# Performance work log

Hardware: AMD Instinct MI355X
Metric: run time of the kernel (lower is better)

The kernel has to match this reference:

```python
import jax, jax.numpy as jnp
import numpy as np

B, S, E, H, D = 4, 2048, 2048, 16, 128
EPS = 1e-6


def _rope_cache(seq_len, dim, base=10000.0):
    # standard rotary cache, half-split layout matching rotate_half
    inv_freq = 1.0 / (base ** (np.arange(0, dim // 2, dtype=np.float32) / (dim // 2)))
    t = np.arange(seq_len, dtype=np.float32)
    freqs = np.outer(t, inv_freq)                     # [S, D/2]
    emb = np.concatenate([freqs, freqs], axis=-1)     # [S, D]
    cos = jnp.asarray(np.cos(emb))[None, :, None, :]  # [1, S, 1, D]
    sin = jnp.asarray(np.sin(emb))[None, :, None, :]
    return cos, sin


def setup_inputs() -> dict:
    key = jax.random.key(0)
    ks = jax.random.split(key, 5)
    scale = 1.0 / np.sqrt(E)
    x = jax.random.normal(ks[0], (B, S, E), dtype=jnp.float32)
    Wq = jax.random.normal(ks[1], (E, E), dtype=jnp.float32) * scale
    Wk = jax.random.normal(ks[2], (E, E), dtype=jnp.float32) * scale
    Wv = jax.random.normal(ks[3], (E, E), dtype=jnp.float32) * scale
    Wo = jax.random.normal(ks[4], (E, E), dtype=jnp.float32) * scale
    cos, sin = _rope_cache(S, D)
    return {"x": x, "cos": cos, "sin": sin, "Wq": Wq, "Wk": Wk, "Wv": Wv, "Wo": Wo}


def _rotate_half(t):
    d = t.shape[-1] // 2
    return jnp.concatenate([-t[..., d:], t[..., :d]], axis=-1)


def _rms_norm(t, eps):
    return t * jax.lax.rsqrt(jnp.mean(t * t, axis=-1, keepdims=True) + eps)


def reference(x, cos, sin, Wq, Wk, Wv, Wo):
    b, s, _ = x.shape
    # QKV projections (Linear without bias: x @ W.T), reshape to heads
    q = (x @ Wq.T).reshape(b, s, H, D)
    k = (x @ Wk.T).reshape(b, s, H, D)
    v = (x @ Wv.T).reshape(b, s, H, D)
    # RoPE then QK RMSNorm (no learned scale)
    q = _rms_norm(q * cos + _rotate_half(q) * sin, EPS)
    k = _rms_norm(k * cos + _rotate_half(k) * sin, EPS)
    # non-causal SDPA
    scores = jnp.einsum("bqhd,bkhd->bhqk", q, k) / np.sqrt(D)
    probs = jax.nn.softmax(scores, axis=-1)
    y = jnp.einsum("bhqk,bkhd->bqhd", probs, v).reshape(b, s, H * D)
    return y @ Wo.T
```

## Files before the change

kernel.cpp:

```cpp
#include <hip/hip_runtime.h>
#include <hip/hip_bf16.h>
#include <math.h>


typedef __bf16 bf16_t;
typedef __bf16 bf16x2 __attribute__((ext_vector_type(2)));
typedef __bf16 bf16x4 __attribute__((ext_vector_type(4)));
typedef __bf16 bf16x8 __attribute__((ext_vector_type(8)));
typedef float f32x2 __attribute__((ext_vector_type(2)));
typedef float f32x4 __attribute__((ext_vector_type(4)));
typedef float f32x16 __attribute__((ext_vector_type(16)));
typedef unsigned int u32;
typedef u32 u32x4 __attribute__((ext_vector_type(4)));

typedef __attribute__((address_space(1))) const void gas_cvoid;
typedef __attribute__((address_space(3))) void las_void;

#define MFMA16(a, b, c) __builtin_amdgcn_mfma_f32_16x16x32_bf16((a), (b), (c), 0, 0, 0)
#define MFMA32(a, b, c) __builtin_amdgcn_mfma_f32_32x32x16_bf16((a), (b), (c), 0, 0, 0)

__device__ __forceinline__ void gload16(const void* g, void* l) {
  __builtin_amdgcn_global_load_lds((gas_cvoid*)g, (las_void*)l, 16, 0, 0);
}
__device__ __forceinline__ void pl32(u32& a, u32& b) {
  asm volatile("v_permlane32_swap_b32 %0, %1" : "+v"(a), "+v"(b));
}
__device__ __forceinline__ float fexp2(float x) {
  float r;
  asm("v_exp_f32 %0, %1" : "=v"(r) : "v"(x));
  return r;
}

__global__ __launch_bounds__(256) void cvt_all(const float* __restrict__ x,
                                               const float* __restrict__ w0,
                                               const float* __restrict__ w1,
                                               const float* __restrict__ w2,
                                               const float* __restrict__ w3,
                                               bf16_t* __restrict__ xo,
                                               bf16_t* __restrict__ o0,
                                               bf16_t* __restrict__ o1,
                                               bf16_t* __restrict__ o2,
                                               bf16_t* __restrict__ o3) {
  const float* in;
  bf16_t* out;
  size_t i;
  if (blockIdx.x < 16384) {
    in = x; out = xo;
    i = ((size_t)blockIdx.x * 256 + threadIdx.x) * 4;
  } else {
    const int which = (blockIdx.x - 16384) >> 12;
    in = which == 0 ? w0 : which == 1 ? w1 : which == 2 ? w2 : w3;
    out = which == 0 ? o0 : which == 1 ? o1 : which == 2 ? o2 : o3;
    i = ((size_t)((blockIdx.x - 16384) & 4095) * 256 + threadIdx.x) * 4;
  }
  f32x4 v = *(const f32x4*)&in[i];
  bf16x4 o;
#pragma unroll
  for (int j = 0; j < 4; ++j) o[j] = (bf16_t)v[j];
  *(bf16x4*)&out[i] = o;
}

__global__ __launch_bounds__(512, 2) void gemm_qkv(const bf16_t* __restrict__ xb,
                                                   const bf16_t* __restrict__ Wq,
                                                   const bf16_t* __restrict__ Wk,
                                                   const bf16_t* __restrict__ Wv,
                                                   bf16_t* __restrict__ Qo,
                                                   bf16_t* __restrict__ Ko,
                                                   bf16_t* __restrict__ Vo) {
  constexpr int K = 2048;
  __shared__ __attribute__((aligned(16))) char lds[131072];
  const int tid = threadIdx.x;
  const int wave = tid >> 6, lane = tid & 63;
  const int seg = blockIdx.x >> 8;
  const int sbid = blockIdx.x & 255;
  const int swz = (sbid & 7) * 32 + (sbid >> 3);
  const int NT = (seg == 2) ? 32 : 8;
  const int m0 = (swz / NT) * 256, n0 = (swz % NT) * 256;
  const bf16_t* A = (seg == 2) ? Wv : xb;
  const bf16_t* Bt = (seg == 0) ? Wq : (seg == 1) ? Wk : xb;
  bf16_t* C = (seg == 0) ? Qo : (seg == 1) ? Ko : Vo;

  const int srow = tid >> 3;
  const int scol = ((tid & 7) ^ (srow & 7)) * 8;
  const bf16_t* aBase = A + (size_t)(m0 + srow) * K + scol;
  const bf16_t* bBase = Bt + (size_t)(n0 + srow) * K + scol;

  const int wm = wave >> 2, wn = wave & 3;
  const int l15 = lane & 15, l4 = lane >> 4;
  const int axor = l15 & 7;
  char* const wdst = lds + wave * 1024;

  f32x4 acc[8][4] = {};

  gload16(bBase, wdst + 32768);
  gload16(bBase + (size_t)64 * K, wdst + 32768 + 8192);
  gload16(bBase + (size_t)128 * K, wdst + 32768 + 16384);
  gload16(bBase + (size_t)192 * K, wdst + 32768 + 24576);
  gload16(aBase, wdst);
  gload16(aBase + (size_t)128 * K, wdst + 16384);
  gload16(aBase + (size_t)64 * K, wdst + 8192);
  gload16(aBase + (size_t)192 * K, wdst + 24576);

  for (int t = 0; t < 32; ++t) {
    const int buf = t & 1, nbuf = buf ^ 1;
    const char* la = lds + buf * 65536 + wm * 16384;
    const char* lb = lds + buf * 65536 + 32768 + (wn >> 1) * 16384 + (wn & 1) * 8192;
    char* const ndst = wdst + nbuf * 65536;
    bf16x8 bF[4][2];
#pragma unroll
    for (int q = 0; q < 4; ++q) {
      if (q == 0) {
        asm volatile("s_waitcnt vmcnt(2)" ::: "memory");
      } else if (q == 2) {
        if (t < 31)
          asm volatile("s_waitcnt vmcnt(4)" ::: "memory");
        else
          asm volatile("s_waitcnt vmcnt(0)" ::: "memory");
      }
      __builtin_amdgcn_s_barrier();

      bf16x8 aF[2][2];
#pragma unroll
      for (int dm = 0; dm < 2; ++dm)
#pragma unroll
        for (int kk = 0; kk < 2; ++kk)
          aF[dm][kk] = *(const bf16x8*)(la + ((q * 2 + dm) * 16 + l15) * 128 +
                                        ((kk * 4 + l4) ^ axor) * 16);
      if (q == 0) {
#pragma unroll
        for (int ni = 0; ni < 4; ++ni)
#pragma unroll
          for (int kk = 0; kk < 2; ++kk)
            bF[ni][kk] = *(const bf16x8*)(lb + (ni * 16 + l15) * 128 +
                                          ((kk * 4 + l4) ^ axor) * 16);
      }
      if (t < 31) {
        const int off = (t + 1) * 64;
        if (q == 0) {
          gload16(bBase + off, ndst + 32768);
          gload16(bBase + (size_t)64 * K + off, ndst + 32768 + 8192);
        } else if (q == 1) {
          gload16(bBase + (size_t)128 * K + off, ndst + 32768 + 16384);
          gload16(bBase + (size_t)192 * K + off, ndst + 32768 + 24576);
        } else if (q == 2) {
          gload16(aBase + off, ndst);
          gload16(aBase + (size_t)128 * K + off, ndst + 16384);
        } else {
          gload16(aBase + (size_t)64 * K + off, ndst + 8192);
          gload16(aBase + (size_t)192 * K + off, ndst + 24576);
        }
      }
      __builtin_amdgcn_s_setprio(1);
#pragma unroll
      for (int kk = 0; kk < 2; ++kk)
#pragma unroll
        for (int dm = 0; dm < 2; ++dm)
#pragma unroll
          for (int ni = 0; ni < 4; ++ni)
            acc[q * 2 + dm][ni] = MFMA16(aF[dm][kk], bF[ni][kk], acc[q * 2 + dm][ni]);
      __builtin_amdgcn_s_setprio(0);
    }
  }

  const int rBase = m0 + wm * 128 + l4 * 4;
  const int cBase = n0 + wn * 64 + l15;
#pragma unroll
  for (int mi = 0; mi < 8; ++mi)
#pragma unroll
    for (int ni = 0; ni < 4; ++ni)
#pragma unroll
      for (int j = 0; j < 4; ++j) {
        const int r = rBase + mi * 16 + j;
        const int c = cBase + ni * 16;
        const bf16_t v = (bf16_t)acc[mi][ni][j];
        if (seg < 2) {
          const int b = r >> 11, s = r & 2047, hh = c >> 7, d = c & 127;
          C[(((size_t)(b * 16 + hh)) * 2048 + s) * 128 + d] = v;
        } else {
          const int hh = r >> 7, dd = r & 127, b = c >> 11, s = c & 2047;
          C[((size_t)(b * 16 + hh) * 128 + dd) * 2048 + s] = v;
        }
      }
}

__global__ __launch_bounds__(512, 2) void gemm_out(const bf16_t* __restrict__ A,
                                                   const bf16_t* __restrict__ Bt,
                                                   float* __restrict__ C) {
  constexpr int K = 2048;
  __shared__ __attribute__((aligned(16))) char lds[131072];
  const int tid = threadIdx.x;
  const int wave = tid >> 6, lane = tid & 63;
  const int bid = blockIdx.x;
  const int swz = (bid & 7) * 32 + (bid >> 3);
  const int m0 = (swz / 8) * 256, n0 = (swz % 8) * 256;

  const int srow = tid >> 3;
  const int scol = ((tid & 7) ^ (srow & 7)) * 8;
  const bf16_t* aBase = A + (size_t)(m0 + srow) * K + scol;
  const bf16_t* bBase = Bt + (size_t)(n0 + srow) * K + scol;

  const int wm = wave >> 2, wn = wave & 3;
  const int l15 = lane & 15, l4 = lane >> 4;
  const int axor = l15 & 7;
  char* const wdst = lds + wave * 1024;

  f32x4 acc[8][4] = {};

  gload16(bBase, wdst + 32768);
  gload16(bBase + (size_t)64 * K, wdst + 32768 + 8192);
  gload16(bBase + (size_t)128 * K, wdst + 32768 + 16384);
  gload16(bBase + (size_t)192 * K, wdst + 32768 + 24576);
  gload16(aBase, wdst);
  gload16(aBase + (size_t)128 * K, wdst + 16384);
  gload16(aBase + (size_t)64 * K, wdst + 8192);
  gload16(aBase + (size_t)192 * K, wdst + 24576);

  for (int t = 0; t < 32; ++t) {
    const int buf = t & 1, nbuf = buf ^ 1;
    const char* la = lds + buf * 65536 + wm * 16384;
    const char* lb = lds + buf * 65536 + 32768 + (wn >> 1) * 16384 + (wn & 1) * 8192;
    char* const ndst = wdst + nbuf * 65536;
    bf16x8 bF[4][2];
#pragma unroll
    for (int q = 0; q < 4; ++q) {
      if (q == 0) {
        asm volatile("s_waitcnt vmcnt(2)" ::: "memory");
      } else if (q == 2) {
        if (t < 31)
          asm volatile("s_waitcnt vmcnt(4)" ::: "memory");
        else
          asm volatile("s_waitcnt vmcnt(0)" ::: "memory");
      }
      __builtin_amdgcn_s_barrier();

      bf16x8 aF[2][2];
#pragma unroll
      for (int dm = 0; dm < 2; ++dm)
#pragma unroll
        for (int kk = 0; kk < 2; ++kk)
          aF[dm][kk] = *(const bf16x8*)(la + ((q * 2 + dm) * 16 + l15) * 128 +
                                        ((kk * 4 + l4) ^ axor) * 16);
      if (q == 0) {
#pragma unroll
        for (int ni = 0; ni < 4; ++ni)
#pragma unroll
          for (int kk = 0; kk < 2; ++kk)
            bF[ni][kk] = *(const bf16x8*)(lb + (ni * 16 + l15) * 128 +
                                          ((kk * 4 + l4) ^ axor) * 16);
      }
      if (t < 31) {
        const int off = (t + 1) * 64;
        if (q == 0) {
          gload16(bBase + off, ndst + 32768);
          gload16(bBase + (size_t)64 * K + off, ndst + 32768 + 8192);
        } else if (q == 1) {
          gload16(bBase + (size_t)128 * K + off, ndst + 32768 + 16384);
          gload16(bBase + (size_t)192 * K + off, ndst + 32768 + 24576);
        } else if (q == 2) {
          gload16(aBase + off, ndst);
          gload16(aBase + (size_t)128 * K + off, ndst + 16384);
        } else {
          gload16(aBase + (size_t)64 * K + off, ndst + 8192);
          gload16(aBase + (size_t)192 * K + off, ndst + 24576);
        }
      }
      __builtin_amdgcn_s_setprio(1);
#pragma unroll
      for (int kk = 0; kk < 2; ++kk)
#pragma unroll
        for (int dm = 0; dm < 2; ++dm)
#pragma unroll
          for (int ni = 0; ni < 4; ++ni)
            acc[q * 2 + dm][ni] = MFMA16(aF[dm][kk], bF[ni][kk], acc[q * 2 + dm][ni]);
      __builtin_amdgcn_s_setprio(0);
    }
  }

  const int rBase = m0 + wm * 128 + l4 * 4;
  const int cBase = n0 + wn * 64 + l15;
#pragma unroll
  for (int mi = 0; mi < 8; ++mi)
#pragma unroll
    for (int ni = 0; ni < 4; ++ni)
#pragma unroll
      for (int j = 0; j < 4; ++j)
        C[(size_t)(rBase + mi * 16 + j) * 2048 + cBase + ni * 16] = acc[mi][ni][j];
}

__global__ __launch_bounds__(256) void rope_rms2(bf16_t* __restrict__ Qb,
                                                 bf16_t* __restrict__ Kb,
                                                 const float* __restrict__ Cs,
                                                 const float* __restrict__ Sn) {
  bf16_t* T = (blockIdx.x >> 12) ? Kb : Qb;
  const int bid = blockIdx.x & 4095;
  const int wave = threadIdx.x >> 6, lane = threadIdx.x & 63;
#pragma unroll 1
  for (int rr = 0; rr < 8; ++rr) {
    const size_t row = (size_t)bid * 32 + wave * 8 + rr;
    const int s = (int)(row & 2047);
    bf16_t* p = &T[row * 128 + 2 * lane];
    const float a0 = (float)p[0], a1 = (float)p[1];
    f32x2 cv = *(const f32x2*)&Cs[(size_t)s * 128 + 2 * lane];
    f32x2 sv = *(const f32x2*)&Sn[(size_t)s * 128 + 2 * lane];
    const float p0 = __shfl_xor(a0, 32);
    const float p1 = __shfl_xor(a1, 32);
    const float sg = (lane < 32) ? -1.f : 1.f;
    const float r0 = a0 * cv.x + sg * p0 * sv.x;
    const float r1 = a1 * cv.y + sg * p1 * sv.y;
    float ss = r0 * r0 + r1 * r1;
#pragma unroll
    for (int off = 1; off < 64; off <<= 1) ss += __shfl_xor(ss, off);
    const float inv = rsqrtf(ss * (1.0f / 128.0f) + 1e-6f);
    p[0] = (bf16_t)(r0 * inv);
    p[1] = (bf16_t)(r1 * inv);
  }
}

__global__ __launch_bounds__(512, 2) void attn_fwd(const bf16_t* __restrict__ Q,
                                                   const bf16_t* __restrict__ K,
                                                   const bf16_t* __restrict__ Vt,
                                                   bf16_t* __restrict__ Y) {
  __shared__ __attribute__((aligned(16))) bf16_t ldsK[2][64 * 128];
  __shared__ __attribute__((aligned(16))) bf16_t ldsV[2][128 * 64];
  const int tid = threadIdx.x, wave = tid >> 6, lane = tid & 63;
  const int l31 = lane & 31, hi = lane >> 5;
  const int pid = blockIdx.x;
  const int bh = (pid & 7) * 8 + ((pid >> 3) & 7);
  const int qb = pid >> 6;
  const int b = bh >> 4, h = bh & 15;
  const bf16_t* Qh = Q + (size_t)bh * 2048 * 128;
  const bf16_t* Kh = K + (size_t)bh * 2048 * 128;
  const bf16_t* Vh = Vt + (size_t)bh * 128 * 2048;
  const int q0 = qb * 256 + wave * 32;

  bf16x8 qf[8];
#pragma unroll
  for (int dk = 0; dk < 8; ++dk)
    qf[dk] = *(const bf16x8*)&Qh[(size_t)(q0 + l31) * 128 + dk * 16 + hi * 8];

  f32x16 ot[4] = {};
  float l_r = 0.f;
  const float SC2 = 0.08838834764831845f * 1.44269504088896341f;
  const float NC2 = -11.5f * 1.44269504088896341f;

  auto stage = [&](int kt, int bu) {
#pragma unroll
    for (int i = 0; i < 2; ++i) {
      const int G = wave * 64 + lane + i * 512;
      char* dstK = (char*)&ldsK[bu][0] + (wave * 64 + i * 512) * 16;
      char* dstV = (char*)&ldsV[bu][0] + (wave * 64 + i * 512) * 16;
      const int kvr = G >> 4, glk = G & 15;
      gload16(Kh + (size_t)(kt * 64 + kvr) * 128 + ((glk ^ (kvr & 7)) * 8), dstK);
      const int dr = G >> 3, glv = G & 7;
      gload16(Vh + (size_t)dr * 2048 + kt * 64 + ((glv ^ (dr & 7)) * 8), dstV);
    }
  };

  stage(0, 0);
  stage(1, 1);
  asm volatile("s_waitcnt vmcnt(4)" ::: "memory");
  __builtin_amdgcn_s_barrier();
  __builtin_amdgcn_sched_barrier(0);

  for (int kt = 0; kt < 32; ++kt) {
    const int bu = kt & 1;
    const int r7 = l31 & 7;

    f32x16 sa0 = {}, sa1 = {};
    __builtin_amdgcn_s_setprio(1);
#pragma unroll
    for (int dk = 0; dk < 8; ++dk) {
      const int g = ((dk << 1) | hi) ^ r7;
      bf16x8 kf0 = *(const bf16x8*)&ldsK[bu][l31 * 128 + g * 8];
      bf16x8 kf1 = *(const bf16x8*)&ldsK[bu][(32 + l31) * 128 + g * 8];
      sa0 = MFMA32(kf0, qf[dk], sa0);
      sa1 = MFMA32(kf1, qf[dk], sa1);
    }
    __builtin_amdgcn_s_setprio(0);

    u32 w[2][8];
    float ssum = 0.f;
#pragma unroll
    for (int i = 0; i < 8; ++i) {
      const float p0 = fexp2(fmaf(sa0[2 * i], SC2, NC2));
      const float p1 = fexp2(fmaf(sa0[2 * i + 1], SC2, NC2));
      const float p2 = fexp2(fmaf(sa1[2 * i], SC2, NC2));
      const float p3 = fexp2(fmaf(sa1[2 * i + 1], SC2, NC2));
      ssum += (p0 + p1) + (p2 + p3);
      bf16x2 t0, t1;
      t0[0] = (bf16_t)p0; t0[1] = (bf16_t)p1;
      t1[0] = (bf16_t)p2; t1[1] = (bf16_t)p3;
      w[0][i] = __builtin_bit_cast(u32, t0);
      w[1][i] = __builtin_bit_cast(u32, t1);
    }
    ssum += __shfl_xor(ssum, 32);
    l_r += ssum;

#pragma unroll
    for (int ks = 0; ks < 4; ++ks) {
      const int tsel = ks >> 1, k4 = (ks & 1) * 4;
      u32 a0 = w[tsel][k4 + 0], b0 = w[tsel][k4 + 2];
      u32 a1 = w[tsel][k4 + 1], b1 = w[tsel][k4 + 3];
      pl32(a0, b0);
      pl32(a1, b1);
      u32x4 fw;
      fw.x = a0; fw.y = a1; fw.z = b0; fw.w = b1;
      const bf16x8 pf = __builtin_bit_cast(bf16x8, fw);
      const int gv = ((ks << 1) | hi) ^ r7;
      __builtin_amdgcn_s_setprio(1);
#pragma unroll
      for (int db = 0; db < 4; ++db) {
        bf16x8 vf = *(const bf16x8*)&ldsV[bu][(db * 32 + l31) * 64 + gv * 8];
        ot[db] = MFMA32(vf, pf, ot[db]);
      }
      __builtin_amdgcn_s_setprio(0);
    }

    __builtin_amdgcn_s_barrier();
    __builtin_amdgcn_sched_barrier(0);
    if (kt < 30) {
      stage(kt + 2, bu);
      asm volatile("s_waitcnt vmcnt(4)" ::: "memory");
    } else {
      asm volatile("s_waitcnt vmcnt(0)" ::: "memory");
    }
    __builtin_amdgcn_s_barrier();
    __builtin_amdgcn_sched_barrier(0);
  }

  const float rl = 1.f / l_r;
  const size_t yrow = ((size_t)(b * 2048 + q0 + l31) * 16 + h) * 128;
#pragma unroll
  for (int db = 0; db < 4; ++db)
#pragma unroll
    for (int g2 = 0; g2 < 4; ++g2) {
      bf16x4 ov;
#pragma unroll
      for (int j = 0; j < 4; ++j) ov[j] = (bf16_t)(ot[db][g2 * 4 + j] * rl);
      *(bf16x4*)&Y[yrow + db * 32 + g2 * 8 + hi * 4] = ov;
    }
}

extern "C" void kernel_launch(void* const* d_in, const int* in_sizes, int n_in,
                              void* d_out, int out_size, void* d_ws, size_t ws_size,
                              hipStream_t stream) {
  const float* x = (const float*)d_in[0];
  const float* cs = (const float*)d_in[1];
  const float* sn = (const float*)d_in[2];
  const float* Wq = (const float*)d_in[3];
  const float* Wk = (const float*)d_in[4];
  const float* Wv = (const float*)d_in[5];
  const float* Wo = (const float*)d_in[6];

  bf16_t* ws = (bf16_t*)d_ws;
  const size_t TSZ = (size_t)4 * 2048 * 2048;
  const size_t WSZ = (size_t)2048 * 2048;
  bf16_t* xb = ws;
  bf16_t* Wqb = ws + TSZ;
  bf16_t* Wkb = Wqb + WSZ;
  bf16_t* Wvb = Wkb + WSZ;
  bf16_t* Wob = Wvb + WSZ;
  bf16_t* Qb = ws + 2 * TSZ;
  bf16_t* Kb = Qb + TSZ;
  bf16_t* Vtb = Kb + TSZ;
  bf16_t* Yb = xb;

  cvt_all<<<32768, 256, 0, stream>>>(x, Wq, Wk, Wv, Wo, xb, Wqb, Wkb, Wvb, Wob);
  gemm_qkv<<<768, 512, 0, stream>>>(xb, Wqb, Wkb, Wvb, Qb, Kb, Vtb);
  rope_rms2<<<8192, 256, 0, stream>>>(Qb, Kb, cs, sn);
  attn_fwd<<<512, 512, 0, stream>>>(Qb, Kb, Vtb, Yb);
  gemm_out<<<256, 512, 0, stream>>>(Yb, Wob, (float*)d_out);
}
```

Measured before the change: 470.9 us.

## Process two query tiles per wave to reuse staged K/V tiles

Each wave now computes two 32-row query tiles against every staged K/V tile, doubling the queries per block and halving the attention grid. This cuts global-to-LDS K/V traffic and barrier overhead per unit of work. It doubles the Q fragments and output accumulators held in registers, risking spills or lower occupancy, and leaves one block per CU.

```diff
diff --git a/kernel.cpp b/kernel.cpp
--- a/kernel.cpp
+++ b/kernel.cpp
@@ -331,15 +331,17 @@
   const bf16_t* Qh = Q + (size_t)bh * 2048 * 128;
   const bf16_t* Kh = K + (size_t)bh * 2048 * 128;
   const bf16_t* Vh = Vt + (size_t)bh * 128 * 2048;
-  const int q0 = qb * 256 + wave * 32;
-
-  bf16x8 qf[8];
-#pragma unroll
-  for (int dk = 0; dk < 8; ++dk)
-    qf[dk] = *(const bf16x8*)&Qh[(size_t)(q0 + l31) * 128 + dk * 16 + hi * 8];
-
-  f32x16 ot[4] = {};
-  float l_r = 0.f;
+  const int q0 = qb * 512 + wave * 32;
+
+  bf16x8 qfA[8], qfB[8];
+#pragma unroll
+  for (int dk = 0; dk < 8; ++dk) {
+    qfA[dk] = *(const bf16x8*)&Qh[(size_t)(q0 + l31) * 128 + dk * 16 + hi * 8];
+    qfB[dk] = *(const bf16x8*)&Qh[(size_t)(q0 + 256 + l31) * 128 + dk * 16 + hi * 8];
+  }
+
+  f32x16 otA[4] = {}, otB[4] = {};
+  float lA = 0.f, lB = 0.f;
   const float SC2 = 0.08838834764831845f * 1.44269504088896341f;
   const float NC2 = -11.5f * 1.44269504088896341f;
 
@@ -356,16 +358,8 @@
     }
   };
 
-  stage(0, 0);
-  stage(1, 1);
-  asm volatile("s_waitcnt vmcnt(4)" ::: "memory");
-  __builtin_amdgcn_s_barrier();
-  __builtin_amdgcn_sched_barrier(0);
-
-  for (int kt = 0; kt < 32; ++kt) {
-    const int bu = kt & 1;
-    const int r7 = l31 & 7;
-
+  auto tile_work = [&](const bf16x8 (&qf)[8], f32x16 (&ot)[4], float& lr,
+                       int bu, int r7) {
     f32x16 sa0 = {}, sa1 = {};
     __builtin_amdgcn_s_setprio(1);
 #pragma unroll
@@ -394,7 +388,7 @@
       w[1][i] = __builtin_bit_cast(u32, t1);
     }
     ssum += __shfl_xor(ssum, 32);
-    l_r += ssum;
+    lr += ssum;
 
 #pragma unroll
     for (int ks = 0; ks < 4; ++ks) {
@@ -415,6 +409,21 @@
       }
       __builtin_amdgcn_s_setprio(0);
     }
+  };
+
+  stage(0, 0);
+  stage(1, 1);
+  asm volatile("s_waitcnt vmcnt(4)" ::: "memory");
+  __builtin_amdgcn_s_barrier();
+  __builtin_amdgcn_sched_barrier(0);
+
+  for (int kt = 0; kt < 32; ++kt) {
+    const int bu = kt & 1;
+    const int r7 = l31 & 7;
+
+    tile_work(qfA, otA, lA, bu, r7);
+    __builtin_amdgcn_sched_barrier(0);
+    tile_work(qfB, otB, lB, bu, r7);
 
     __builtin_amdgcn_s_barrier();
     __builtin_amdgcn_sched_barrier(0);
@@ -428,16 +437,21 @@
     __builtin_amdgcn_sched_barrier(0);
   }
 
-  const float rl = 1.f / l_r;
-  const size_t yrow = ((size_t)(b * 2048 + q0 + l31) * 16 + h) * 128;
+  const float rlA = 1.f / lA, rlB = 1.f / lB;
+  const size_t yrA = ((size_t)(b * 2048 + q0 + l31) * 16 + h) * 128;
+  const size_t yrB = ((size_t)(b * 2048 + q0 + 256 + l31) * 16 + h) * 128;
 #pragma unroll
   for (int db = 0; db < 4; ++db)
 #pragma unroll
     for (int g2 = 0; g2 < 4; ++g2) {
-      bf16x4 ov;
-#pragma unroll
-      for (int j = 0; j < 4; ++j) ov[j] = (bf16_t)(ot[db][g2 * 4 + j] * rl);
-      *(bf16x4*)&Y[yrow + db * 32 + g2 * 8 + hi * 4] = ov;
+      bf16x4 ovA, ovB;
+#pragma unroll
+      for (int j = 0; j < 4; ++j) {
+        ovA[j] = (bf16_t)(otA[db][g2 * 4 + j] * rlA);
+        ovB[j] = (bf16_t)(otB[db][g2 * 4 + j] * rlB);
+      }
+      *(bf16x4*)&Y[yrA + db * 32 + g2 * 8 + hi * 4] = ovA;
+      *(bf16x4*)&Y[yrB + db * 32 + g2 * 8 + hi * 4] = ovB;
     }
 }
 
@@ -468,6 +482,6 @@
   cvt_all<<<32768, 256, 0, stream>>>(x, Wq, Wk, Wv, Wo, xb, Wqb, Wkb, Wvb, Wob);
   gemm_qkv<<<768, 512, 0, stream>>>(xb, Wqb, Wkb, Wvb, Qb, Kb, Vtb);
   rope_rms2<<<8192, 256, 0, stream>>>(Qb, Kb, cs, sn);
-  attn_fwd<<<512, 512, 0, stream>>>(Qb, Kb, Vtb, Yb);
+  attn_fwd<<<256, 512, 0, stream>>>(Qb, Kb, Vtb, Yb);
   gemm_out<<<256, 512, 0, stream>>>(Yb, Wob, (float*)d_out);
 }
```

New measurement: 622.4 us. 1.32x slower.
